# Optimization experiments

Hardware: AMD Instinct MI355X
Metric: run time of the kernel (lower is better)

The kernel has to match this reference:

```python
import jax, jax.numpy as jnp
import numpy as np
import math

# Constants matching init_kwargs
H = 16            # num_attention_heads
K = 8             # tisa_num_kernels
NUM_AGNOSTIC = 2  # num_position_agnostic_heads
MAX_FV = 512.0
MIN_FV = 8.0
P_EPS = 1e-8
EPS = 1e-8


def _slopes():
    # ALiBi-like geometric slope schedule from the module __init__ (non-learned buffer)
    first = -math.log(P_EPS) / (MIN_FV / 2.0)
    last = -math.log(P_EPS) / (MAX_FV / 2.0)
    aware = H - NUM_AGNOSTIC
    s = first * (last / first) ** (jnp.arange(H, dtype=jnp.float32) / (aware - 1))
    # position-agnostic heads get zero slope
    return s * (jnp.arange(H) < aware).astype(jnp.float32)


def setup_inputs() -> dict:
    key = jax.random.key(0)
    ks = jax.random.split(key, 5)
    B, L, D = 4, 1024, 64
    q = jax.random.normal(ks[0], (B, H, L, D), jnp.float32)
    k = jax.random.normal(ks[1], (B, H, L, D), jnp.float32)
    v = jax.random.normal(ks[2], (B, H, L, D), jnp.float32)
    offsets = jax.random.normal(ks[3], (1, K, H, 1, 1), jnp.float32) * 15.0
    amplitudes = jax.random.normal(ks[4], (1, K, H, 1, 1), jnp.float32) * 0.01
    sharpness = jnp.full((1, K, H, 1, 1), 5.0, jnp.float32)
    bias_param = jnp.ones((1, H, 1, 1), jnp.float32)
    return {"q": q, "k": k, "v": v, "offsets": offsets, "amplitudes": amplitudes,
            "sharpness": sharpness, "bias_param": bias_param}


def reference(q, k, v, offsets, amplitudes, sharpness, bias_param):
    B, Hh, L, D = q.shape
    rel = jnp.arange(-L + 1, L, dtype=q.dtype)            # (2L-1,) relative positions
    slopes = _slopes()                                     # (H,)
    exp_decay = -jnp.abs(rel)[None, :] * slopes[:, None]   # (H, 2L-1)

    off = offsets.reshape(K, Hh, 1)
    amp = amplitudes.reshape(K, Hh, 1)
    sh = sharpness.reshape(K, Hh, 1)
    # sigmoid kernel per (kernel, head, relpos); eval mode -> no dropout
    kernel = jnp.abs(amp) * jax.nn.sigmoid(jnp.sign(amp) * ((rel[None, None, :] - off) / sh))
    ksum = kernel.sum(axis=0)                              # (H, 2L-1)
    bias_rel = jnp.log(ksum + EPS + bias_param.reshape(Hh, 1))
    rel_bias = bias_rel + exp_decay                        # (H, 2L-1)

    # relative -> absolute: bias[i, j] = rel_bias[j - i + L - 1]
    idx = jnp.arange(L)[None, :] - jnp.arange(L)[:, None] + (L - 1)  # (L, L)
    attn_bias = rel_bias[:, idx]                           # (H, L, L)

    scale = 1.0 / jnp.sqrt(jnp.asarray(D, q.dtype))
    scores = jnp.einsum('bhqd,bhkd->bhqk', q, k) * scale + attn_bias[None]
    probs = jax.nn.softmax(scores, axis=-1)
    return jnp.einsum('bhqk,bhkd->bhqd', probs, v)
```

## Files before the change

### kernel.cpp

```cpp
#include <hip/hip_runtime.h>
#include <math.h>

#define Bq 4
#define Hh 16
#define Lq 1024
#define Dd 64
#define Kk 8
#define QT 128
#define KT 128
#define SRk 72
#define SRv 136
#define TB 1152
#define FMAX 8.0f
#define LOG2E 1.44269504f

typedef __attribute__((ext_vector_type(8))) short short8;
typedef __attribute__((ext_vector_type(4))) unsigned int u32x4;
typedef __attribute__((ext_vector_type(16))) float f32x16;

__device__ __forceinline__ unsigned int pk2(float a, float b) {
    return __builtin_amdgcn_perm(__float_as_uint(b) + 0x8000u,
                                 __float_as_uint(a) + 0x8000u,
                                 0x07060302u);
}

__device__ __forceinline__ int jperm(int j) {
    return (j & 32) | ((j & 8) << 1) | ((j & 4) << 1) | ((j & 16) >> 2) | (j & 3);
}

__global__ __launch_bounds__(256, 2) void attn_kernel(
    const float* __restrict__ qp, const float* __restrict__ kp,
    const float* __restrict__ vp,
    const float* __restrict__ off, const float* __restrict__ amp,
    const float* __restrict__ sh, const float* __restrict__ bpar,
    float* __restrict__ out)
{
    __shared__ __align__(16) short k_s[KT * SRk];
    __shared__ __align__(16) short v_s[Dd * SRv];
    __shared__ __align__(16) float bias4[4 * TB];
    __shared__ float l_s[QT];

    const int bh = blockIdx.x;
    const int qs = blockIdx.y * QT;
    const int t  = threadIdx.x;
    const int w  = t >> 6;
    const int lane = t & 63;
    const int l31 = lane & 31;
    const int h5  = lane >> 5;
    const int h   = bh & 15;

    float slope = (h < Hh - 2) ? 4.605170185988092f * exp2f(-6.0f * (float)h / 13.0f) : 0.0f;
    #pragma unroll
    for (int it = 0; it < 5; ++it) {
        int i = it * 256 + t;
        if (i < TB - 1) {
            float rel = (float)(i - 127 - qs);
            float ksum = 0.0f;
            #pragma unroll
            for (int kk = 0; kk < Kk; ++kk) {
                float a = amp[kk * Hh + h];
                float o = off[kk * Hh + h];
                float s = sh[kk * Hh + h];
                float sgn = (a > 0.0f) ? 1.0f : ((a < 0.0f) ? -1.0f : 0.0f);
                ksum += fabsf(a) / (1.0f + __expf(-sgn * (rel - o) / s));
            }
            bias4[i] = (logf(ksum + 1e-8f + bpar[h]) - fabsf(rel) * slope - FMAX) * LOG2E;
        }
    }

    const float QS = 0.125f * LOG2E;
    short8 bq[4];
    const float* qrow = qp + ((size_t)bh * Lq + qs + 32 * w + l31) * Dd;
    #pragma unroll
    for (int c = 0; c < 4; ++c) {
        float4 x0 = *(const float4*)(qrow + c * 16 + h5 * 8);
        float4 x1 = *(const float4*)(qrow + c * 16 + h5 * 8 + 4);
        u32x4 a;
        a[0] = pk2(x0.x * QS, x0.y * QS);
        a[1] = pk2(x0.z * QS, x0.w * QS);
        a[2] = pk2(x1.x * QS, x1.y * QS);
        a[3] = pk2(x1.z * QS, x1.w * QS);
        bq[c] = __builtin_bit_cast(short8, a);
    }

    const int g  = t >> 4;
    const int cl = t & 15;
    const int j0 = 4 * g;
    const int c4 = 4 * cl;
    const int vcb[2] = { jperm(j0), 64 + jperm(j0) };
    const float* kbase = kp + (size_t)bh * Lq * Dd;
    const float* vbase = vp + (size_t)bh * Lq * Dd;

    float4 kr[2][4], vr[2][4];
    #pragma unroll
    for (int s = 0; s < 2; ++s)
        #pragma unroll
        for (int u = 0; u < 4; ++u) {
            kr[s][u] = *(const float4*)(kbase + (size_t)(64 * s + j0 + u) * Dd + c4);
            vr[s][u] = *(const float4*)(vbase + (size_t)(64 * s + j0 + u) * Dd + c4);
        }

    __syncthreads();

    #pragma unroll
    for (int it = 0; it < 5; ++it) {
        int i = it * 256 + t;
        if (i < TB) {
            float b1 = bias4[i + 1 <= TB - 2 ? i + 1 : TB - 2];
            float b2 = bias4[i + 2 <= TB - 2 ? i + 2 : TB - 2];
            float b3 = bias4[i + 3 <= TB - 2 ? i + 3 : TB - 2];
            bias4[TB + i]     = b1;
            bias4[2 * TB + i] = b2;
            bias4[3 * TB + i] = b3;
        }
    }
    #pragma unroll
    for (int s = 0; s < 2; ++s) {
        #pragma unroll
        for (int u = 0; u < 4; ++u) {
            uint2 kv;
            kv.x = pk2(kr[s][u].x, kr[s][u].y);
            kv.y = pk2(kr[s][u].z, kr[s][u].w);
            *(uint2*)&k_s[(64 * s + j0 + u) * SRk + c4] = kv;
        }
        #pragma unroll
        for (int cc = 0; cc < 4; ++cc) {
            int d = c4 + cc;
            uint2 vv;
            vv.x = pk2(((const float*)&vr[s][0])[cc], ((const float*)&vr[s][1])[cc]);
            vv.y = pk2(((const float*)&vr[s][2])[cc], ((const float*)&vr[s][3])[cc]);
            *(uint2*)&v_s[d * SRv + (vcb[s] ^ (8 * ((d >> 3) & 7)))] = vv;
        }
    }
    __syncthreads();

    f32x16 O0, O1;
    #pragma unroll
    for (int r = 0; r < 16; ++r) { O0[r] = 0.f; O1[r] = 0.f; }
    float l_part = 0.0f;

    const int L0 = 4 * h5 - 32 * w - l31 + 127;
    const int phi = L0 & 3;
    const float* bcopy = bias4 + phi * TB - phi;

    #pragma unroll 1
    for (int kt = 0; kt < Lq / KT; ++kt) {
        const int ks = kt * KT;

        if (kt < 7) {
            const float* kn = kbase + (size_t)(ks + KT) * Dd;
            const float* vn = vbase + (size_t)(ks + KT) * Dd;
            #pragma unroll
            for (int s = 0; s < 2; ++s)
                #pragma unroll
                for (int u = 0; u < 4; ++u) {
                    kr[s][u] = *(const float4*)(kn + (size_t)(64 * s + j0 + u) * Dd + c4);
                    vr[s][u] = *(const float4*)(vn + (size_t)(64 * s + j0 + u) * Dd + c4);
                }
        }

        #pragma unroll
        for (int s = 0; s < 2; ++s) {
            f32x16 S0, S1;
            #pragma unroll
            for (int r = 0; r < 16; ++r) { S0[r] = 0.f; S1[r] = 0.f; }
            #pragma unroll
            for (int c = 0; c < 4; ++c) {
                short8 ak0 = *(const short8*)&k_s[(64 * s + l31) * SRk + c * 16 + h5 * 8];
                S0 = __builtin_amdgcn_mfma_f32_32x32x16_bf16(ak0, bq[c], S0, 0, 0, 0);
            }
            #pragma unroll
            for (int c = 0; c < 4; ++c) {
                short8 ak1 = *(const short8*)&k_s[(64 * s + 32 + l31) * SRk + c * 16 + h5 * 8];
                S1 = __builtin_amdgcn_mfma_f32_32x32x16_bf16(ak1, bq[c], S1, 0, 0, 0);
            }

            float lsum = 0.0f;
            #pragma unroll
            for (int p = 0; p < 4; ++p) {
                int base0 = ks + 64 * s + 8 * p + L0;
                float4 b0 = *(const float4*)(bcopy + base0);
                float4 b1 = *(const float4*)(bcopy + base0 + 32);
                #pragma unroll
                for (int q = 0; q < 4; ++q) {
                    int r = 4 * p + q;
                    float bq0 = (q == 0) ? b0.x : (q == 1) ? b0.y : (q == 2) ? b0.z : b0.w;
                    float bq1 = (q == 0) ? b1.x : (q == 1) ? b1.y : (q == 2) ? b1.z : b1.w;
                    float e0 = __builtin_amdgcn_exp2f(S0[r] + bq0);
                    float e1 = __builtin_amdgcn_exp2f(S1[r] + bq1);
                    S0[r] = e0; S1[r] = e1;
                    lsum += e0 + e1;
                }
            }
            l_part += lsum;

            short8 ap[4];
            #pragma unroll
            for (int c = 0; c < 4; ++c) {
                int b = (c & 1) * 4;
                u32x4 a;
                if (c >> 1) {
                    a[0] = pk2(S1[b + 0], S1[b + 1]);
                    a[1] = pk2(S1[b + 2], S1[b + 3]);
                    a[2] = pk2(S1[b + 8], S1[b + 9]);
                    a[3] = pk2(S1[b + 10], S1[b + 11]);
                } else {
                    a[0] = pk2(S0[b + 0], S0[b + 1]);
                    a[1] = pk2(S0[b + 2], S0[b + 3]);
                    a[2] = pk2(S0[b + 8], S0[b + 9]);
                    a[3] = pk2(S0[b + 10], S0[b + 11]);
                }
                ap[c] = __builtin_bit_cast(short8, a);
            }

            #pragma unroll
            for (int nb = 0; nb < 2; ++nb) {
                int d = nb * 32 + l31;
                int swz = 8 * ((d >> 3) & 7);
                f32x16 acc = nb ? O1 : O0;
                #pragma unroll
                for (int c = 0; c < 4; ++c) {
                    short8 bv = *(const short8*)&v_s[d * SRv + 64 * s + ((c * 16 + h5 * 8) ^ swz)];
                    acc = __builtin_amdgcn_mfma_f32_32x32x16_bf16(ap[c], bv, acc, 0, 0, 0);
                }
                if (nb) O1 = acc; else O0 = acc;
            }
        }

        __syncthreads();
        if (kt < 7) {
            #pragma unroll
            for (int s = 0; s < 2; ++s) {
                #pragma unroll
                for (int u = 0; u < 4; ++u) {
                    uint2 kv;
                    kv.x = pk2(kr[s][u].x, kr[s][u].y);
                    kv.y = pk2(kr[s][u].z, kr[s][u].w);
                    *(uint2*)&k_s[(64 * s + j0 + u) * SRk + c4] = kv;
                }
                #pragma unroll
                for (int cc = 0; cc < 4; ++cc) {
                    int d = c4 + cc;
                    uint2 vv;
                    vv.x = pk2(((const float*)&vr[s][0])[cc], ((const float*)&vr[s][1])[cc]);
                    vv.y = pk2(((const float*)&vr[s][2])[cc], ((const float*)&vr[s][3])[cc]);
                    *(uint2*)&v_s[d * SRv + (vcb[s] ^ (8 * ((d >> 3) & 7)))] = vv;
                }
            }
        }
        __syncthreads();
    }

    float l = l_part;
    l += __shfl_xor(l, 32);
    l_s[32 * w + l31] = 1.0f / l;
    float* ob = out + ((size_t)bh * Lq + qs) * Dd;
    #pragma unroll
    for (int r = 0; r < 16; ++r) {
        int rowp = (r & 3) + 8 * (r >> 2) + 4 * h5;
        float inv = l_s[32 * w + rowp];
        ob[(size_t)(32 * w + rowp) * Dd + l31]      = O0[r] * inv;
        ob[(size_t)(32 * w + rowp) * Dd + 32 + l31] = O1[r] * inv;
    }
}

extern "C" void kernel_launch(void* const* d_in, const int* in_sizes, int n_in,
                              void* d_out, int out_size, void* d_ws, size_t ws_size,
                              hipStream_t stream) {
    const float* q   = (const float*)d_in[0];
    const float* k   = (const float*)d_in[1];
    const float* v   = (const float*)d_in[2];
    const float* off = (const float*)d_in[3];
    const float* amp = (const float*)d_in[4];
    const float* sh  = (const float*)d_in[5];
    const float* bp  = (const float*)d_in[6];
    float* out = (float*)d_out;

    dim3 grid(Bq * Hh, Lq / QT);
    attn_kernel<<<grid, 256, 0, stream>>>(q, k, v, off, amp, sh, bp, out);
}
```

Baseline: 124.9 us.

## Split key tile across wave pairs with 512-thread blocks and reduce partial outputs

Doubles the block to 512 threads so each pair of waves shares one 32-row query slice, with each wave handling half of every 128-key tile instead of one wave looping over both halves. Partial O accumulators and row sums are combined through shared memory at the end, reusing the K/V/bias LDS region. The aim is more waves per CU to hide MFMA and exp latency and halve the serial work per wave. The cost is an extra cross-wave reduction and more register/LDS pressure, which could limit occupancy under the 512x2 launch bound.

Measured after the change: 128.8 us. +3.1%, slower.

```diff
diff --git a/kernel.cpp b/kernel.cpp
--- a/kernel.cpp
+++ b/kernel.cpp
@@ -14,6 +14,11 @@
 #define FMAX 8.0f
 #define LOG2E 1.44269504f
 
+#define KSZ (KT * SRk * 2)
+#define VSZ (Dd * SRv * 2)
+#define BOFF (KSZ + VSZ)
+#define SMEM_BYTES (BOFF + 4 * TB * 4)
+
 typedef __attribute__((ext_vector_type(8))) short short8;
 typedef __attribute__((ext_vector_type(4))) unsigned int u32x4;
 typedef __attribute__((ext_vector_type(16))) float f32x16;
@@ -28,22 +33,24 @@
     return (j & 32) | ((j & 8) << 1) | ((j & 4) << 1) | ((j & 16) >> 2) | (j & 3);
 }
 
-__global__ __launch_bounds__(256, 2) void attn_kernel(
+__global__ __launch_bounds__(512, 2) void attn_kernel(
     const float* __restrict__ qp, const float* __restrict__ kp,
     const float* __restrict__ vp,
     const float* __restrict__ off, const float* __restrict__ amp,
     const float* __restrict__ sh, const float* __restrict__ bpar,
     float* __restrict__ out)
 {
-    __shared__ __align__(16) short k_s[KT * SRk];
-    __shared__ __align__(16) short v_s[Dd * SRv];
-    __shared__ __align__(16) float bias4[4 * TB];
-    __shared__ float l_s[QT];
+    __shared__ __align__(16) char smem[SMEM_BYTES];
+    short* k_s   = (short*)smem;
+    short* v_s   = (short*)(smem + KSZ);
+    float* bias4 = (float*)(smem + BOFF);
 
     const int bh = blockIdx.x;
     const int qs = blockIdx.y * QT;
     const int t  = threadIdx.x;
     const int w  = t >> 6;
+    const int qw = w >> 1;
+    const int sw = w & 1;
     const int lane = t & 63;
     const int l31 = lane & 31;
     const int h5  = lane >> 5;
@@ -51,8 +58,8 @@
 
     float slope = (h < Hh - 2) ? 4.605170185988092f * exp2f(-6.0f * (float)h / 13.0f) : 0.0f;
     #pragma unroll
-    for (int it = 0; it < 5; ++it) {
-        int i = it * 256 + t;
+    for (int it = 0; it < 3; ++it) {
+        int i = it * 512 + t;
         if (i < TB - 1) {
             float rel = (float)(i - 127 - qs);
             float ksum = 0.0f;
@@ -70,7 +77,7 @@
 
     const float QS = 0.125f * LOG2E;
     short8 bq[4];
-    const float* qrow = qp + ((size_t)bh * Lq + qs + 32 * w + l31) * Dd;
+    const float* qrow = qp + ((size_t)bh * Lq + qs + 32 * qw + l31) * Dd;
     #pragma unroll
     for (int c = 0; c < 4; ++c) {
         float4 x0 = *(const float4*)(qrow + c * 16 + h5 * 8);
@@ -85,26 +92,24 @@
 
     const int g  = t >> 4;
     const int cl = t & 15;
-    const int j0 = 4 * g;
     const int c4 = 4 * cl;
-    const int vcb[2] = { jperm(j0), 64 + jperm(j0) };
+    const int jrow = 4 * g;
+    const int vcb = 64 * (g >> 4) + jperm(jrow & 63);
     const float* kbase = kp + (size_t)bh * Lq * Dd;
     const float* vbase = vp + (size_t)bh * Lq * Dd;
 
-    float4 kr[2][4], vr[2][4];
-    #pragma unroll
-    for (int s = 0; s < 2; ++s)
-        #pragma unroll
-        for (int u = 0; u < 4; ++u) {
-            kr[s][u] = *(const float4*)(kbase + (size_t)(64 * s + j0 + u) * Dd + c4);
-            vr[s][u] = *(const float4*)(vbase + (size_t)(64 * s + j0 + u) * Dd + c4);
-        }
+    float4 kr[4], vr[4];
+    #pragma unroll
+    for (int u = 0; u < 4; ++u) {
+        kr[u] = *(const float4*)(kbase + (size_t)(jrow + u) * Dd + c4);
+        vr[u] = *(const float4*)(vbase + (size_t)(jrow + u) * Dd + c4);
+    }
 
     __syncthreads();
 
     #pragma unroll
-    for (int it = 0; it < 5; ++it) {
-        int i = it * 256 + t;
+    for (int it = 0; it < 3; ++it) {
+        int i = it * 512 + t;
         if (i < TB) {
             float b1 = bias4[i + 1 <= TB - 2 ? i + 1 : TB - 2];
             float b2 = bias4[i + 2 <= TB - 2 ? i + 2 : TB - 2];
@@ -115,22 +120,19 @@
         }
     }
     #pragma unroll
-    for (int s = 0; s < 2; ++s) {
-        #pragma unroll
-        for (int u = 0; u < 4; ++u) {
-            uint2 kv;
-            kv.x = pk2(kr[s][u].x, kr[s][u].y);
-            kv.y = pk2(kr[s][u].z, kr[s][u].w);
-            *(uint2*)&k_s[(64 * s + j0 + u) * SRk + c4] = kv;
-        }
-        #pragma unroll
-        for (int cc = 0; cc < 4; ++cc) {
-            int d = c4 + cc;
-            uint2 vv;
-            vv.x = pk2(((const float*)&vr[s][0])[cc], ((const float*)&vr[s][1])[cc]);
-            vv.y = pk2(((const float*)&vr[s][2])[cc], ((const float*)&vr[s][3])[cc]);
-            *(uint2*)&v_s[d * SRv + (vcb[s] ^ (8 * ((d >> 3) & 7)))] = vv;
-        }
+    for (int u = 0; u < 4; ++u) {
+        uint2 kv;
+        kv.x = pk2(kr[u].x, kr[u].y);
+        kv.y = pk2(kr[u].z, kr[u].w);
+        *(uint2*)&k_s[(jrow + u) * SRk + c4] = kv;
+    }
+    #pragma unroll
+    for (int cc = 0; cc < 4; ++cc) {
+        int d = c4 + cc;
+        uint2 vv;
+        vv.x = pk2(((const float*)&vr[0])[cc], ((const float*)&vr[1])[cc]);
+        vv.y = pk2(((const float*)&vr[2])[cc], ((const float*)&vr[3])[cc]);
+        *(uint2*)&v_s[d * SRv + (vcb ^ (8 * ((d >> 3) & 7)))] = vv;
     }
     __syncthreads();
 
@@ -139,7 +141,7 @@
     for (int r = 0; r < 16; ++r) { O0[r] = 0.f; O1[r] = 0.f; }
     float l_part = 0.0f;
 
-    const int L0 = 4 * h5 - 32 * w - l31 + 127;
+    const int L0 = 4 * h5 - 32 * qw - l31 + 127;
     const int phi = L0 & 3;
     const float* bcopy = bias4 + phi * TB - phi;
 
@@ -151,116 +153,114 @@
             const float* kn = kbase + (size_t)(ks + KT) * Dd;
             const float* vn = vbase + (size_t)(ks + KT) * Dd;
             #pragma unroll
-            for (int s = 0; s < 2; ++s)
-                #pragma unroll
-                for (int u = 0; u < 4; ++u) {
-                    kr[s][u] = *(const float4*)(kn + (size_t)(64 * s + j0 + u) * Dd + c4);
-                    vr[s][u] = *(const float4*)(vn + (size_t)(64 * s + j0 + u) * Dd + c4);
-                }
-        }
-
-        #pragma unroll
-        for (int s = 0; s < 2; ++s) {
-            f32x16 S0, S1;
-            #pragma unroll
-            for (int r = 0; r < 16; ++r) { S0[r] = 0.f; S1[r] = 0.f; }
+            for (int u = 0; u < 4; ++u) {
+                kr[u] = *(const float4*)(kn + (size_t)(jrow + u) * Dd + c4);
+                vr[u] = *(const float4*)(vn + (size_t)(jrow + u) * Dd + c4);
+            }
+        }
+
+        f32x16 S0, S1;
+        #pragma unroll
+        for (int r = 0; r < 16; ++r) { S0[r] = 0.f; S1[r] = 0.f; }
+        #pragma unroll
+        for (int c = 0; c < 4; ++c) {
+            short8 ak0 = *(const short8*)&k_s[(64 * sw + l31) * SRk + c * 16 + h5 * 8];
+            S0 = __builtin_amdgcn_mfma_f32_32x32x16_bf16(ak0, bq[c], S0, 0, 0, 0);
+        }
+        #pragma unroll
+        for (int c = 0; c < 4; ++c) {
+            short8 ak1 = *(const short8*)&k_s[(64 * sw + 32 + l31) * SRk + c * 16 + h5 * 8];
+            S1 = __builtin_amdgcn_mfma_f32_32x32x16_bf16(ak1, bq[c], S1, 0, 0, 0);
+        }
+
+        float lsum = 0.0f;
+        #pragma unroll
+        for (int p = 0; p < 4; ++p) {
+            int base0 = ks + 64 * sw + 8 * p + L0;
+            float4 b0 = *(const float4*)(bcopy + base0);
+            float4 b1 = *(const float4*)(bcopy + base0 + 32);
+            #pragma unroll
+            for (int q = 0; q < 4; ++q) {
+                int r = 4 * p + q;
+                float bq0 = (q == 0) ? b0.x : (q == 1) ? b0.y : (q == 2) ? b0.z : b0.w;
+                float bq1 = (q == 0) ? b1.x : (q == 1) ? b1.y : (q == 2) ? b1.z : b1.w;
+                float e0 = __builtin_amdgcn_exp2f(S0[r] + bq0);
+                float e1 = __builtin_amdgcn_exp2f(S1[r] + bq1);
+                S0[r] = e0; S1[r] = e1;
+                lsum += e0 + e1;
+            }
+        }
+        l_part += lsum;
+
+        short8 ap[4];
+        #pragma unroll
+        for (int c = 0; c < 4; ++c) {
+            int b = (c & 1) * 4;
+            u32x4 a;
+            if (c >> 1) {
+                a[0] = pk2(S1[b + 0], S1[b + 1]);
+                a[1] = pk2(S1[b + 2], S1[b + 3]);
+                a[2] = pk2(S1[b + 8], S1[b + 9]);
+                a[3] = pk2(S1[b + 10], S1[b + 11]);
+            } else {
+                a[0] = pk2(S0[b + 0], S0[b + 1]);
+                a[1] = pk2(S0[b + 2], S0[b + 3]);
+                a[2] = pk2(S0[b + 8], S0[b + 9]);
+                a[3] = pk2(S0[b + 10], S0[b + 11]);
+            }
+            ap[c] = __builtin_bit_cast(short8, a);
+        }
+
+        #pragma unroll
+        for (int nb = 0; nb < 2; ++nb) {
+            int d = nb * 32 + l31;
+            int swz = 8 * ((d >> 3) & 7);
+            f32x16 acc = nb ? O1 : O0;
             #pragma unroll
             for (int c = 0; c < 4; ++c) {
-                short8 ak0 = *(const short8*)&k_s[(64 * s + l31) * SRk + c * 16 + h5 * 8];
-                S0 = __builtin_amdgcn_mfma_f32_32x32x16_bf16(ak0, bq[c], S0, 0, 0, 0);
-            }
-            #pragma unroll
-            for (int c = 0; c < 4; ++c) {
-                short8 ak1 = *(const short8*)&k_s[(64 * s + 32 + l31) * SRk + c * 16 + h5 * 8];
-                S1 = __builtin_amdgcn_mfma_f32_32x32x16_bf16(ak1, bq[c], S1, 0, 0, 0);
-            }
-
-            float lsum = 0.0f;
-            #pragma unroll
-            for (int p = 0; p < 4; ++p) {
-                int base0 = ks + 64 * s + 8 * p + L0;
-                float4 b0 = *(const float4*)(bcopy + base0);
-                float4 b1 = *(const float4*)(bcopy + base0 + 32);
-                #pragma unroll
-                for (int q = 0; q < 4; ++q) {
-                    int r = 4 * p + q;
-                    float bq0 = (q == 0) ? b0.x : (q == 1) ? b0.y : (q == 2) ? b0.z : b0.w;
-                    float bq1 = (q == 0) ? b1.x : (q == 1) ? b1.y : (q == 2) ? b1.z : b1.w;
-                    float e0 = __builtin_amdgcn_exp2f(S0[r] + bq0);
-                    float e1 = __builtin_amdgcn_exp2f(S1[r] + bq1);
-                    S0[r] = e0; S1[r] = e1;
-                    lsum += e0 + e1;
-                }
-            }
-            l_part += lsum;
-
-            short8 ap[4];
-            #pragma unroll
-            for (int c = 0; c < 4; ++c) {
-                int b = (c & 1) * 4;
-                u32x4 a;
-                if (c >> 1) {
-                    a[0] = pk2(S1[b + 0], S1[b + 1]);
-                    a[1] = pk2(S1[b + 2], S1[b + 3]);
-                    a[2] = pk2(S1[b + 8], S1[b + 9]);
-                    a[3] = pk2(S1[b + 10], S1[b + 11]);
-                } else {
-                    a[0] = pk2(S0[b + 0], S0[b + 1]);
-                    a[1] = pk2(S0[b + 2], S0[b + 3]);
-                    a[2] = pk2(S0[b + 8], S0[b + 9]);
-                    a[3] = pk2(S0[b + 10], S0[b + 11]);
-                }
-                ap[c] = __builtin_bit_cast(short8, a);
-            }
-
-            #pragma unroll
-            for (int nb = 0; nb < 2; ++nb) {
-                int d = nb * 32 + l31;
-                int swz = 8 * ((d >> 3) & 7);
-                f32x16 acc = nb ? O1 : O0;
-                #pragma unroll
-                for (int c = 0; c < 4; ++c) {
-                    short8 bv = *(const short8*)&v_s[d * SRv + 64 * s + ((c * 16 + h5 * 8) ^ swz)];
-                    acc = __builtin_amdgcn_mfma_f32_32x32x16_bf16(ap[c], bv, acc, 0, 0, 0);
-                }
-                if (nb) O1 = acc; else O0 = acc;
-            }
+                short8 bv = *(const short8*)&v_s[d * SRv + 64 * sw + ((c * 16 + h5 * 8) ^ swz)];
+                acc = __builtin_amdgcn_mfma_f32_32x32x16_bf16(ap[c], bv, acc, 0, 0, 0);
+            }
+            if (nb) O1 = acc; else O0 = acc;
         }
 
         __syncthreads();
         if (kt < 7) {
             #pragma unroll
-            for (int s = 0; s < 2; ++s) {
-                #pragma unroll
-                for (int u = 0; u < 4; ++u) {
-                    uint2 kv;
-                    kv.x = pk2(kr[s][u].x, kr[s][u].y);
-                    kv.y = pk2(kr[s][u].z, kr[s][u].w);
-                    *(uint2*)&k_s[(64 * s + j0 + u) * SRk + c4] = kv;
-                }
-                #pragma unroll
-                for (int cc = 0; cc < 4; ++cc) {
-                    int d = c4 + cc;
-                    uint2 vv;
-                    vv.x = pk2(((const float*)&vr[s][0])[cc], ((const float*)&vr[s][1])[cc]);
-                    vv.y = pk2(((const float*)&vr[s][2])[cc], ((const float*)&vr[s][3])[cc]);
-                    *(uint2*)&v_s[d * SRv + (vcb[s] ^ (8 * ((d >> 3) & 7)))] = vv;
-                }
+            for (int u = 0; u < 4; ++u) {
+                uint2 kv;
+                kv.x = pk2(kr[u].x, kr[u].y);
+                kv.y = pk2(kr[u].z, kr[u].w);
+                *(uint2*)&k_s[(jrow + u) * SRk + c4] = kv;
+            }
+            #pragma unroll
+            for (int cc = 0; cc < 4; ++cc) {
+                int d = c4 + cc;
+                uint2 vv;
+                vv.x = pk2(((const float*)&vr[0])[cc], ((const float*)&vr[1])[cc]);
+                vv.y = pk2(((const float*)&vr[2])[cc], ((const float*)&vr[3])[cc]);
+                *(uint2*)&v_s[d * SRv + (vcb ^ (8 * ((d >> 3) & 7)))] = vv;
             }
         }
         __syncthreads();
     }
 
-    float l = l_part;
-    l += __shfl_xor(l, 32);
-    l_s[32 * w + l31] = 1.0f / l;
-    float* ob = out + ((size_t)bh * Lq + qs) * Dd;
+    l_part += __shfl_xor(l_part, 32);
+    float* red = (float*)smem;
+    const int rb = (w * 64 + lane) * 17;
+    #pragma unroll
+    for (int r = 0; r < 16; ++r) red[rb + r] = sw ? O0[r] : O1[r];
+    red[rb + 16] = l_part;
+    __syncthreads();
+    const int pb = ((w ^ 1) * 64 + lane) * 17;
+    float inv = 1.0f / (l_part + red[pb + 16]);
+    float* ob = out + ((size_t)bh * Lq + qs + 32 * qw) * Dd;
     #pragma unroll
     for (int r = 0; r < 16; ++r) {
+        float o = (sw ? O1[r] : O0[r]) + red[pb + r];
         int rowp = (r & 3) + 8 * (r >> 2) + 4 * h5;
-        float inv = l_s[32 * w + rowp];
-        ob[(size_t)(32 * w + rowp) * Dd + l31]      = O0[r] * inv;
-        ob[(size_t)(32 * w + rowp) * Dd + 32 + l31] = O1[r] * inv;
+        float invp = __shfl(inv, rowp, 32);
+        ob[(size_t)rowp * Dd + 32 * sw + l31] = o * invp;
     }
 }
 
@@ -277,5 +277,5 @@
     float* out = (float*)d_out;
 
     dim3 grid(Bq * Hh, Lq / QT);
-    attn_kernel<<<grid, 256, 0, stream>>>(q, k, v, off, amp, sh, bp, out);
-}
+    attn_kernel<<<grid, 512, 0, stream>>>(q, k, v, off, amp, sh, bp, out);
+}
```

## Seed QK MFMA with bias, compute row sums via MFMA, use hardware bf16 pack

Applied to the files above, without the earlier changes.

The QK accumulators are initialised with the bias values, so the MFMA adds the bias and the separate add is dropped. The softmax denominator is now computed by an extra MFMA of the bf16 probabilities against a ones vector. This replaces the scalar lsum reduction, the cross-lane shuffle and the LDS l_s buffer. Float-to-bf16 packing uses the native v_cvt_pk_bf16_f32 instruction instead of the perm-based rounding, and s_setprio is raised around the MFMA blocks. The row sum now uses bf16-rounded probabilities and adds four MFMAs per step.

Result: faster. 122.2 us (-2.2%).

```diff
diff --git a/kernel.cpp b/kernel.cpp
--- a/kernel.cpp
+++ b/kernel.cpp
@@ -24,6 +24,12 @@
                                  0x07060302u);
 }
 
+__device__ __forceinline__ unsigned int cvtpk(float a, float b) {
+    unsigned int r;
+    asm("v_cvt_pk_bf16_f32 %0, %1, %2" : "=v"(r) : "v"(a), "v"(b));
+    return r;
+}
+
 __device__ __forceinline__ int jperm(int j) {
     return (j & 32) | ((j & 8) << 1) | ((j & 4) << 1) | ((j & 16) >> 2) | (j & 3);
 }
@@ -38,7 +44,6 @@
     __shared__ __align__(16) short k_s[KT * SRk];
     __shared__ __align__(16) short v_s[Dd * SRv];
     __shared__ __align__(16) float bias4[4 * TB];
-    __shared__ float l_s[QT];
 
     const int bh = blockIdx.x;
     const int qs = blockIdx.y * QT;
@@ -119,25 +124,27 @@
         #pragma unroll
         for (int u = 0; u < 4; ++u) {
             uint2 kv;
-            kv.x = pk2(kr[s][u].x, kr[s][u].y);
-            kv.y = pk2(kr[s][u].z, kr[s][u].w);
+            kv.x = cvtpk(kr[s][u].x, kr[s][u].y);
+            kv.y = cvtpk(kr[s][u].z, kr[s][u].w);
             *(uint2*)&k_s[(64 * s + j0 + u) * SRk + c4] = kv;
         }
         #pragma unroll
         for (int cc = 0; cc < 4; ++cc) {
             int d = c4 + cc;
             uint2 vv;
-            vv.x = pk2(((const float*)&vr[s][0])[cc], ((const float*)&vr[s][1])[cc]);
-            vv.y = pk2(((const float*)&vr[s][2])[cc], ((const float*)&vr[s][3])[cc]);
+            vv.x = cvtpk(((const float*)&vr[s][0])[cc], ((const float*)&vr[s][1])[cc]);
+            vv.y = cvtpk(((const float*)&vr[s][2])[cc], ((const float*)&vr[s][3])[cc]);
             *(uint2*)&v_s[d * SRv + (vcb[s] ^ (8 * ((d >> 3) & 7)))] = vv;
         }
     }
     __syncthreads();
 
-    f32x16 O0, O1;
-    #pragma unroll
-    for (int r = 0; r < 16; ++r) { O0[r] = 0.f; O1[r] = 0.f; }
-    float l_part = 0.0f;
+    f32x16 O0, O1, Lacc;
+    #pragma unroll
+    for (int r = 0; r < 16; ++r) { O0[r] = 0.f; O1[r] = 0.f; Lacc[r] = 0.f; }
+    short8 ones;
+    #pragma unroll
+    for (int e = 0; e < 8; ++e) ones[e] = (short)0x3F80;
 
     const int L0 = 4 * h5 - 32 * w - l31 + 127;
     const int phi = L0 & 3;
@@ -162,37 +169,35 @@
         #pragma unroll
         for (int s = 0; s < 2; ++s) {
             f32x16 S0, S1;
-            #pragma unroll
-            for (int r = 0; r < 16; ++r) { S0[r] = 0.f; S1[r] = 0.f; }
-            #pragma unroll
-            for (int c = 0; c < 4; ++c) {
-                short8 ak0 = *(const short8*)&k_s[(64 * s + l31) * SRk + c * 16 + h5 * 8];
-                S0 = __builtin_amdgcn_mfma_f32_32x32x16_bf16(ak0, bq[c], S0, 0, 0, 0);
-            }
-            #pragma unroll
-            for (int c = 0; c < 4; ++c) {
-                short8 ak1 = *(const short8*)&k_s[(64 * s + 32 + l31) * SRk + c * 16 + h5 * 8];
-                S1 = __builtin_amdgcn_mfma_f32_32x32x16_bf16(ak1, bq[c], S1, 0, 0, 0);
-            }
-
-            float lsum = 0.0f;
             #pragma unroll
             for (int p = 0; p < 4; ++p) {
                 int base0 = ks + 64 * s + 8 * p + L0;
                 float4 b0 = *(const float4*)(bcopy + base0);
                 float4 b1 = *(const float4*)(bcopy + base0 + 32);
-                #pragma unroll
-                for (int q = 0; q < 4; ++q) {
-                    int r = 4 * p + q;
-                    float bq0 = (q == 0) ? b0.x : (q == 1) ? b0.y : (q == 2) ? b0.z : b0.w;
-                    float bq1 = (q == 0) ? b1.x : (q == 1) ? b1.y : (q == 2) ? b1.z : b1.w;
-                    float e0 = __builtin_amdgcn_exp2f(S0[r] + bq0);
-                    float e1 = __builtin_amdgcn_exp2f(S1[r] + bq1);
-                    S0[r] = e0; S1[r] = e1;
-                    lsum += e0 + e1;
-                }
-            }
-            l_part += lsum;
+                S0[4 * p + 0] = b0.x; S0[4 * p + 1] = b0.y;
+                S0[4 * p + 2] = b0.z; S0[4 * p + 3] = b0.w;
+                S1[4 * p + 0] = b1.x; S1[4 * p + 1] = b1.y;
+                S1[4 * p + 2] = b1.z; S1[4 * p + 3] = b1.w;
+            }
+
+            __builtin_amdgcn_s_setprio(1);
+            #pragma unroll
+            for (int c = 0; c < 4; ++c) {
+                short8 ak0 = *(const short8*)&k_s[(64 * s + l31) * SRk + c * 16 + h5 * 8];
+                S0 = __builtin_amdgcn_mfma_f32_32x32x16_bf16(ak0, bq[c], S0, 0, 0, 0);
+            }
+            #pragma unroll
+            for (int c = 0; c < 4; ++c) {
+                short8 ak1 = *(const short8*)&k_s[(64 * s + 32 + l31) * SRk + c * 16 + h5 * 8];
+                S1 = __builtin_amdgcn_mfma_f32_32x32x16_bf16(ak1, bq[c], S1, 0, 0, 0);
+            }
+            __builtin_amdgcn_s_setprio(0);
+
+            #pragma unroll
+            for (int r = 0; r < 16; ++r) {
+                S0[r] = __builtin_amdgcn_exp2f(S0[r]);
+                S1[r] = __builtin_amdgcn_exp2f(S1[r]);
+            }
 
             short8 ap[4];
             #pragma unroll
@@ -200,19 +205,20 @@
                 int b = (c & 1) * 4;
                 u32x4 a;
                 if (c >> 1) {
-                    a[0] = pk2(S1[b + 0], S1[b + 1]);
-                    a[1] = pk2(S1[b + 2], S1[b + 3]);
-                    a[2] = pk2(S1[b + 8], S1[b + 9]);
-                    a[3] = pk2(S1[b + 10], S1[b + 11]);
+                    a[0] = cvtpk(S1[b + 0], S1[b + 1]);
+                    a[1] = cvtpk(S1[b + 2], S1[b + 3]);
+                    a[2] = cvtpk(S1[b + 8], S1[b + 9]);
+                    a[3] = cvtpk(S1[b + 10], S1[b + 11]);
                 } else {
-                    a[0] = pk2(S0[b + 0], S0[b + 1]);
-                    a[1] = pk2(S0[b + 2], S0[b + 3]);
-                    a[2] = pk2(S0[b + 8], S0[b + 9]);
-                    a[3] = pk2(S0[b + 10], S0[b + 11]);
+                    a[0] = cvtpk(S0[b + 0], S0[b + 1]);
+                    a[1] = cvtpk(S0[b + 2], S0[b + 3]);
+                    a[2] = cvtpk(S0[b + 8], S0[b + 9]);
+                    a[3] = cvtpk(S0[b + 10], S0[b + 11]);
                 }
                 ap[c] = __builtin_bit_cast(short8, a);
             }
 
+            __builtin_amdgcn_s_setprio(1);
             #pragma unroll
             for (int nb = 0; nb < 2; ++nb) {
                 int d = nb * 32 + l31;
@@ -225,6 +231,10 @@
                 }
                 if (nb) O1 = acc; else O0 = acc;
             }
+            #pragma unroll
+            for (int c = 0; c < 4; ++c)
+                Lacc = __builtin_amdgcn_mfma_f32_32x32x16_bf16(ap[c], ones, Lacc, 0, 0, 0);
+            __builtin_amdgcn_s_setprio(0);
         }
 
         __syncthreads();
@@ -234,16 +244,16 @@
                 #pragma unroll
                 for (int u = 0; u < 4; ++u) {
                     uint2 kv;
-                    kv.x = pk2(kr[s][u].x, kr[s][u].y);
-                    kv.y = pk2(kr[s][u].z, kr[s][u].w);
+                    kv.x = cvtpk(kr[s][u].x, kr[s][u].y);
+                    kv.y = cvtpk(kr[s][u].z, kr[s][u].w);
                     *(uint2*)&k_s[(64 * s + j0 + u) * SRk + c4] = kv;
                 }
                 #pragma unroll
                 for (int cc = 0; cc < 4; ++cc) {
                     int d = c4 + cc;
                     uint2 vv;
-                    vv.x = pk2(((const float*)&vr[s][0])[cc], ((const float*)&vr[s][1])[cc]);
-                    vv.y = pk2(((const float*)&vr[s][2])[cc], ((const float*)&vr[s][3])[cc]);
+                    vv.x = cvtpk(((const float*)&vr[s][0])[cc], ((const float*)&vr[s][1])[cc]);
+                    vv.y = cvtpk(((const float*)&vr[s][2])[cc], ((const float*)&vr[s][3])[cc]);
                     *(uint2*)&v_s[d * SRv + (vcb[s] ^ (8 * ((d >> 3) & 7)))] = vv;
                 }
             }
@@ -251,14 +261,11 @@
         __syncthreads();
     }
 
-    float l = l_part;
-    l += __shfl_xor(l, 32);
-    l_s[32 * w + l31] = 1.0f / l;
     float* ob = out + ((size_t)bh * Lq + qs) * Dd;
     #pragma unroll
     for (int r = 0; r < 16; ++r) {
         int rowp = (r & 3) + 8 * (r >> 2) + 4 * h5;
-        float inv = l_s[32 * w + rowp];
+        float inv = 1.0f / Lacc[r];
         ob[(size_t)(32 * w + rowp) * Dd + l31]      = O0[r] * inv;
         ob[(size_t)(32 * w + rowp) * Dd + 32 + l31] = O1[r] * inv;
     }
```
